# Performance work log

Measured on AMD Instinct MI355X. Metric: run time of the kernel, lower is better.

The kernel has to match this reference:

```python
import jax, jax.numpy as jnp
import numpy as np

B, S, H, I, E, TOP_K = 1, 2048, 1024, 4096, 8, 1


def setup_inputs() -> dict:
    key = jax.random.key(0)
    ks = jax.random.split(key, 8)
    s = 0.02  # init scale for weights
    return {
        "hidden_states": jax.random.normal(ks[0], (B, S, H), jnp.float32),
        "router_w": jax.random.normal(ks[1], (E, H), jnp.float32) * s,
        "w_gate": jax.random.normal(ks[2], (E, I, H), jnp.float32) * s,
        "w_up": jax.random.normal(ks[3], (E, I, H), jnp.float32) * s,
        "w_down": jax.random.normal(ks[4], (E, H, I), jnp.float32) * s,
        "ws_gate": jax.random.normal(ks[5], (I, H), jnp.float32) * s,
        "ws_up": jax.random.normal(ks[6], (I, H), jnp.float32) * s,
        "ws_down": jax.random.normal(ks[7], (H, I), jnp.float32) * s,
    }


def _mlp(x, wg, wu, wd):
    # silu(x @ Wg^T) * (x @ Wu^T) @ Wd^T  (Llama4TextMLP)
    return (jax.nn.silu(x @ wg.T) * (x @ wu.T)) @ wd.T


def reference(hidden_states, router_w, w_gate, w_up, w_down, ws_gate, ws_up, ws_down):
    b, s, h = hidden_states.shape
    hs = hidden_states.reshape(-1, h)                      # [T, H]
    T = hs.shape[0]
    logits = hs @ router_w.T                               # [T, E]
    top_v, top_i = jax.lax.top_k(logits, TOP_K)            # [T, K]
    masked = jnp.full_like(logits, -jnp.inf)
    masked = masked.at[jnp.arange(T)[:, None], top_i].set(top_v)
    scores = jax.nn.sigmoid(masked)                        # [T, E]; sigmoid(-inf)=0

    # In this module every expert sees ALL tokens, scaled by its (mostly-zero) score.
    routed = scores.T[:, :, None] * hs[None, :, :]         # [E, T, H]

    out = _mlp(hs, ws_gate, ws_up, ws_down)                # shared expert, [T, H]
    gate = jnp.einsum('eth,eih->eti', routed, w_gate)      # [E, T, I]
    up = jnp.einsum('eth,eih->eti', routed, w_up)          # [E, T, I]
    expert_out = jnp.einsum('eti,ehi->eth', jax.nn.silu(gate) * up, w_down)
    out = out + expert_out.sum(axis=0)                     # [T, H]
    return out, scores.T                                   # router_scores is [E, T]
```

## Files before the change

### kernel.cpp

```cpp
#include <hip/hip_runtime.h>
#include <hip/hip_bf16.h>
#include <math.h>

#define T_TOK 2048
#define HDIM 1024
#define IDIM 4096
#define NEXP 8
#define RROWS 3200
#define AROWS 5248
#define ZROW  5120
#define NP2   24
#define BK 32

typedef unsigned int uint;
typedef unsigned short ushort;
typedef __attribute__((ext_vector_type(4))) float f32x4;
typedef __attribute__((ext_vector_type(8))) short bf16x8;

__device__ __forceinline__ ushort f2bf(float f) {
  union { float f; uint u; } c; c.f = f;
  uint u = c.u;
  return (ushort)((u + 0x7FFFu + ((u >> 16) & 1u)) >> 16);
}
__device__ __forceinline__ uint cvtpk(float a, float b) {
  uint r;
  asm("v_cvt_pk_bf16_f32 %0, %1, %2" : "=v"(r) : "v"(a), "v"(b));
  return r;
}
__device__ __forceinline__ void gld16(ushort* lds, const ushort* g) {
  __builtin_amdgcn_global_load_lds(
      (const __attribute__((address_space(1))) uint*)g,
      (__attribute__((address_space(3))) uint*)lds, 16, 0, 0);
}
__device__ __forceinline__ int soff(int row, int kc) {
  return ((row >> 4) << 9) + (kc << 7) + ((row & 15) << 3);
}

#define SYNCV(N) { \
  __builtin_amdgcn_sched_barrier(0); \
  asm volatile("s_waitcnt vmcnt(" #N ") lgkmcnt(0)" ::: "memory"); \
  __builtin_amdgcn_s_barrier(); \
  __builtin_amdgcn_sched_barrier(0); }

__global__ __launch_bounds__(256) void router_kernel(
    const float* __restrict__ hs, const float* __restrict__ rw,
    ushort* __restrict__ Xall, float* __restrict__ scores_out,
    int* __restrict__ eidx, float* __restrict__ sval)
{
  const int wave = threadIdx.x >> 6;
  const int lane = threadIdx.x & 63;
  const int t = blockIdx.x * 4 + wave;
  const float* row = hs + (size_t)t * HDIM;
  float v[16];
  #pragma unroll
  for (int i = 0; i < 16; ++i) {
    v[i] = row[lane + 64 * i];
    Xall[(size_t)t * HDIM + lane + 64 * i] = f2bf(v[i]);
  }
  float logit[8];
  #pragma unroll
  for (int e = 0; e < 8; ++e) {
    const float* wr = rw + e * HDIM;
    float s = 0.f;
    #pragma unroll
    for (int i = 0; i < 16; ++i) s += v[i] * wr[lane + 64 * i];
    #pragma unroll
    for (int off = 32; off; off >>= 1) s += __shfl_xor(s, off, 64);
    logit[e] = s;
  }
  if (lane == 0) {
    int be = 0; float bv = logit[0];
    #pragma unroll
    for (int e = 1; e < 8; ++e) if (logit[e] > bv) { bv = logit[e]; be = e; }
    float sc = 1.f / (1.f + expf(-bv));
    eidx[t] = be; sval[t] = sc;
    #pragma unroll
    for (int e = 0; e < 8; ++e) scores_out[(size_t)e * T_TOK + t] = (e == be) ? sc : 0.f;
  }
}

__global__ __launch_bounds__(256) void plan_kernel(
    const int* __restrict__ eidx, int* __restrict__ row2tok, int4* __restrict__ pairs)
{
  __shared__ int cnt[8];
  __shared__ int slot[8];
  const int tid = threadIdx.x;
  if (tid < 8) cnt[tid] = 0;
  __syncthreads();
  for (int t = tid; t < T_TOK; t += 256) atomicAdd(&cnt[eidx[t]], 1);
  __syncthreads();
  if (tid == 0) {
    int np = 0;
    for (int i = 0; i < 8; ++i) pairs[np++] = make_int4(i * 256, i * 256 + 128, -1, 1);
    int o = 0;
    for (int e = 0; e < 8; ++e) {
      slot[e] = o;
      int cap = (cnt[e] + 127) & ~127;
      int nt = cap / 128;
      for (int j = 0; j < nt; j += 2) {
        int ra = T_TOK + o + j * 128;
        int rb = (j + 1 < nt) ? ra + 128 : ZROW;
        pairs[np++] = make_int4(ra, rb, e, 1);
      }
      o += cap;
    }
    for (; np < NP2; ++np) pairs[np] = make_int4(ZROW, ZROW, 0, 0);
  }
  for (int r = tid; r < RROWS; r += 256) row2tok[r] = -1;
  __syncthreads();
  for (int t = tid; t < T_TOK; t += 256) {
    int e = eidx[t];
    int s = atomicAdd(&slot[e], 1);
    row2tok[s] = t;
  }
}

__global__ __launch_bounds__(256) void gather_kernel(
    const float* __restrict__ hs, const int* __restrict__ row2tok,
    const float* __restrict__ sval, ushort* __restrict__ Xall)
{
  const int r = blockIdx.x;
  const int t = row2tok[r];
  const int c0 = threadIdx.x * 4;
  ushort4 o;
  if (t >= 0) {
    const float sc = sval[t];
    float4 v = *(const float4*)(hs + (size_t)t * HDIM + c0);
    o.x = f2bf(sc * v.x); o.y = f2bf(sc * v.y); o.z = f2bf(sc * v.z); o.w = f2bf(sc * v.w);
  } else { o.x = o.y = o.z = o.w = 0; }
  *(ushort4*)(Xall + (size_t)(T_TOK + r) * HDIM + c0) = o;
}

#define LOADB1(S, k0) { \
  gr##S = *(const float4*)(gptr + (k0)); \
  ur##S = *(const float4*)(uptr + (k0)); }

#define WRITEB1(S, B) { \
  *(uint2*)&Bg[B][woff] = make_uint2(cvtpk(gr##S.x, gr##S.y), cvtpk(gr##S.z, gr##S.w)); \
  *(uint2*)&Bu[B][woff] = make_uint2(cvtpk(ur##S.x, ur##S.y), cvtpk(ur##S.z, ur##S.w)); }

#define STAGEA(B, k0) { gld16(&As[B][alds0], asrc0 + (k0)); }

#define READ1(B) \
  bf16x8 af[4], gf[2], uf[2]; \
  _Pragma("unroll") \
  for (int m = 0; m < 4; ++m) af[m] = *(const bf16x8*)&As[B][(wm*4+m)*512 + lp]; \
  _Pragma("unroll") \
  for (int n = 0; n < 2; ++n) { \
    gf[n] = *(const bf16x8*)&Bg[B][(wn*2+n)*512 + lp]; \
    uf[n] = *(const bf16x8*)&Bu[B][(wn*2+n)*512 + lp]; }

#define MFMA1 \
  _Pragma("unroll") \
  for (int m = 0; m < 4; ++m) { \
    _Pragma("unroll") \
    for (int n = 0; n < 2; ++n) { \
      accg[m][n] = __builtin_amdgcn_mfma_f32_16x16x32_bf16(af[m], gf[n], accg[m][n], 0, 0, 0); \
      accu[m][n] = __builtin_amdgcn_mfma_f32_16x16x32_bf16(af[m], uf[n], accu[m][n], 0, 0, 0); } }

__global__ __launch_bounds__(1024, 1) void gemm1_kernel(
    const ushort* __restrict__ Xall,
    const float* __restrict__ w_gate, const float* __restrict__ w_up,
    const float* __restrict__ ws_gate, const float* __restrict__ ws_up,
    const int4* __restrict__ pairs, ushort* __restrict__ actall)
{
  __shared__ __align__(16) ushort As[2][8192];
  __shared__ __align__(16) ushort Bg[2][4096];
  __shared__ __align__(16) ushort Bu[2][4096];

  const int b0 = blockIdx.x;
  const int j = b0 & 7, s = b0 >> 3;
  const int panel = j + 8 * (s / NP2);
  const int4 td = pairs[s % NP2];
  if (td.w == 0) return;
  const int r0a = td.x, r0b = td.y, e = td.z;
  const float* __restrict__ gbase = (e < 0) ? ws_gate : w_gate + (size_t)e * IDIM * HDIM;
  const float* __restrict__ ubase = (e < 0) ? ws_up   : w_up   + (size_t)e * IDIM * HDIM;
  const int col0 = panel * 128;

  const int tid = threadIdx.x;
  const int lane = tid & 63;
  const int w = tid >> 6;
  const int wm = w >> 2, wn = w & 3;

  const int brow = tid >> 3, bch = tid & 7;
  const float* gptr = gbase + (size_t)(col0 + brow) * HDIM + bch * 4;
  const float* uptr = ubase + (size_t)(col0 + brow) * HDIM + bch * 4;
  const int woff = soff(brow, bch >> 1) + (bch & 1) * 4;

  const size_t abs0 = (w < 8) ? (size_t)(r0a + w * 16 + (lane & 15))
                              : (size_t)(r0b + (w - 8) * 16 + (lane & 15));
  const ushort* asrc0 = Xall + abs0 * HDIM + (lane >> 4) * 8;
  const int alds0 = w * 512 + lane * 8;

  float4 gr0, ur0, gr1, ur1;
  const int lp = (lane >> 4) * 128 + (lane & 15) * 8;
  f32x4 accg[4][2] = {};
  f32x4 accu[4][2] = {};

  STAGEA(0, 0);
  __builtin_amdgcn_sched_barrier(0);
  LOADB1(0, 0);
  WRITEB1(0, 0);
  LOADB1(1, BK);
  SYNCV(2);

  const int NS = HDIM / BK;
  for (int kk = 0; kk < NS / 2 - 1; ++kk) {
    const int k = kk * 2;
    {
      READ1(0);
      STAGEA(1, (k + 1) * BK);
      __builtin_amdgcn_sched_barrier(0);
      WRITEB1(1, 1);
      LOADB1(0, (k + 2) * BK);
      MFMA1;
      SYNCV(2);
    }
    {
      READ1(1);
      STAGEA(0, (k + 2) * BK);
      __builtin_amdgcn_sched_barrier(0);
      WRITEB1(0, 0);
      LOADB1(1, (k + 3) * BK);
      MFMA1;
      SYNCV(2);
    }
  }
  {
    READ1(0);
    STAGEA(1, (NS - 1) * BK);
    __builtin_amdgcn_sched_barrier(0);
    WRITEB1(1, 1);
    MFMA1;
    SYNCV(0);
  }
  {
    READ1(1);
    MFMA1;
  }

  const int prbase = wm * 64 + ((lane >> 4) << 2);
  const int cbase = col0 + wn * 32 + (lane & 15);
  #pragma unroll
  for (int m = 0; m < 4; ++m)
    #pragma unroll
    for (int n = 0; n < 2; ++n)
      #pragma unroll
      for (int j2 = 0; j2 < 4; ++j2) {
        const int pr = prbase + m * 16 + j2;
        const size_t ar = (wm < 2) ? (size_t)(r0a + pr) : (size_t)(r0b + pr - 128);
        float g = accg[m][n][j2];
        float u = accu[m][n][j2];
        float sv = g / (1.f + __expf(-g)) * u;
        actall[ar * IDIM + cbase + n * 16] = f2bf(sv);
      }
}

#define LOADB2(S, k0) { br##S = *(const float4*)(bptr + (k0)); }

#define WRITEB2(S, B) { \
  *(uint2*)&Bs[B][woff] = make_uint2(cvtpk(br##S.x, br##S.y), cvtpk(br##S.z, br##S.w)); }

#define READ2(B) \
  bf16x8 af[4], bfr[2]; \
  _Pragma("unroll") \
  for (int m = 0; m < 4; ++m) af[m] = *(const bf16x8*)&As[B][(wm*4+m)*512 + lp]; \
  _Pragma("unroll") \
  for (int n = 0; n < 2; ++n) bfr[n] = *(const bf16x8*)&Bs[B][(wn*2+n)*512 + lp];

#define MFMA2 \
  _Pragma("unroll") \
  for (int m = 0; m < 4; ++m) { \
    _Pragma("unroll") \
    for (int n = 0; n < 2; ++n) \
      acc[m][n] = __builtin_amdgcn_mfma_f32_16x16x32_bf16(af[m], bfr[n], acc[m][n], 0, 0, 0); }

__global__ __launch_bounds__(1024, 1) void gemm2_kernel(
    const ushort* __restrict__ actall,
    const float* __restrict__ w_down, const float* __restrict__ ws_down,
    const int4* __restrict__ pairs, const int* __restrict__ row2tok,
    float* __restrict__ out, float* __restrict__ bufr)
{
  __shared__ __align__(16) ushort As[2][8192];
  __shared__ __align__(16) ushort Bs[2][4096];

  const int b0 = blockIdx.x;
  const int panel = b0 & 7;
  const int4 td = pairs[b0 >> 3];
  if (td.w == 0) return;
  const int r0a = td.x, r0b = td.y, e = td.z;
  const float* __restrict__ bbase = (e < 0) ? ws_down : w_down + (size_t)e * HDIM * IDIM;
  const int col0 = panel * 128;

  const int tid = threadIdx.x;
  const int lane = tid & 63;
  const int w = tid >> 6;
  const int wm = w >> 2, wn = w & 3;

  const int brow = tid >> 3, bch = tid & 7;
  const float* bptr = bbase + (size_t)(col0 + brow) * IDIM + bch * 4;
  const int woff = soff(brow, bch >> 1) + (bch & 1) * 4;

  const size_t abs0 = (w < 8) ? (size_t)(r0a + w * 16 + (lane & 15))
                              : (size_t)(r0b + (w - 8) * 16 + (lane & 15));
  const ushort* asrc0 = actall + abs0 * IDIM + (lane >> 4) * 8;
  const int alds0 = w * 512 + lane * 8;

  float4 br0, br1;
  const int lp = (lane >> 4) * 128 + (lane & 15) * 8;
  f32x4 acc[4][2] = {};

  STAGEA(0, 0);
  __builtin_amdgcn_sched_barrier(0);
  LOADB2(0, 0);
  WRITEB2(0, 0);
  LOADB2(1, BK);
  SYNCV(1);

  const int NS = IDIM / BK;
  for (int kk = 0; kk < NS / 2 - 1; ++kk) {
    const int k = kk * 2;
    {
      READ2(0);
      STAGEA(1, (k + 1) * BK);
      __builtin_amdgcn_sched_barrier(0);
      WRITEB2(1, 1);
      LOADB2(0, (k + 2) * BK);
      MFMA2;
      SYNCV(1);
    }
    {
      READ2(1);
      STAGEA(0, (k + 2) * BK);
      __builtin_amdgcn_sched_barrier(0);
      WRITEB2(0, 0);
      LOADB2(1, (k + 3) * BK);
      MFMA2;
      SYNCV(1);
    }
  }
  {
    READ2(0);
    STAGEA(1, (NS - 1) * BK);
    __builtin_amdgcn_sched_barrier(0);
    WRITEB2(1, 1);
    MFMA2;
    SYNCV(0);
  }
  {
    READ2(1);
    MFMA2;
  }

  const int prbase = wm * 64 + ((lane >> 4) << 2);
  const int cbase = col0 + wn * 32 + (lane & 15);
  #pragma unroll
  for (int m = 0; m < 4; ++m)
    #pragma unroll
    for (int j2 = 0; j2 < 4; ++j2) {
      const int pr = prbase + m * 16 + j2;
      const int ar = (wm < 2) ? (r0a + pr) : (r0b + pr - 128);
      if (e < 0) {
        #pragma unroll
        for (int n = 0; n < 2; ++n)
          out[(size_t)ar * HDIM + cbase + n * 16] = acc[m][n][j2];
      } else {
        const int t = row2tok[ar - T_TOK];
        if (t >= 0) {
          #pragma unroll
          for (int n = 0; n < 2; ++n)
            bufr[(size_t)t * HDIM + cbase + n * 16] = acc[m][n][j2];
        }
      }
    }
}

__global__ __launch_bounds__(256) void add_kernel(
    float* __restrict__ out, const float* __restrict__ bufr)
{
  const size_t i = ((size_t)blockIdx.x * 256 + threadIdx.x) * 4;
  float4 a = *(float4*)(out + i);
  const float4 b = *(const float4*)(bufr + i);
  a.x += b.x; a.y += b.y; a.z += b.z; a.w += b.w;
  *(float4*)(out + i) = a;
}

extern "C" void kernel_launch(void* const* d_in, const int* in_sizes, int n_in,
                              void* d_out, int out_size, void* d_ws, size_t ws_size,
                              hipStream_t stream)
{
  const float* hs      = (const float*)d_in[0];
  const float* rw      = (const float*)d_in[1];
  const float* w_gate  = (const float*)d_in[2];
  const float* w_up    = (const float*)d_in[3];
  const float* w_down  = (const float*)d_in[4];
  const float* ws_gate = (const float*)d_in[5];
  const float* ws_up   = (const float*)d_in[6];
  const float* ws_down = (const float*)d_in[7];

  float* out = (float*)d_out;
  float* scores_out = out + (size_t)T_TOK * HDIM;

  char* ws = (char*)d_ws;
  ushort* Xall   = (ushort*)ws;
  ushort* actall = (ushort*)(ws + 10747904);
  float*  bufr   = (float*)(ws + 53739520);
  int*    eidx   = (int*)(ws + 62128128);
  float*  sval   = (float*)(ws + 62136320);
  int*    r2t    = (int*)(ws + 62144512);
  int4*   pairs  = (int4*)(ws + 62157312);

  router_kernel<<<T_TOK / 4, 256, 0, stream>>>(hs, rw, Xall, scores_out, eidx, sval);
  plan_kernel<<<1, 256, 0, stream>>>(eidx, r2t, pairs);
  gather_kernel<<<RROWS, 256, 0, stream>>>(hs, r2t, sval, Xall);
  gemm1_kernel<<<(IDIM / 128) * NP2, 1024, 0, stream>>>(
      Xall, w_gate, w_up, ws_gate, ws_up, pairs, actall);
  gemm2_kernel<<<(HDIM / 128) * NP2, 1024, 0, stream>>>(
      actall, w_down, ws_down, pairs, r2t, out, bufr);
  add_kernel<<<(T_TOK * HDIM) / 1024, 256, 0, stream>>>(out, bufr);
}
```

Baseline: 329.1 us.

## Triple-buffer A tiles in LDS and prefetch two stages ahead

```diff
diff --git a/kernel.cpp b/kernel.cpp
--- a/kernel.cpp
+++ b/kernel.cpp
@@ -139,12 +139,12 @@
   *(uint2*)&Bg[B][woff] = make_uint2(cvtpk(gr##S.x, gr##S.y), cvtpk(gr##S.z, gr##S.w)); \
   *(uint2*)&Bu[B][woff] = make_uint2(cvtpk(ur##S.x, ur##S.y), cvtpk(ur##S.z, ur##S.w)); }
 
-#define STAGEA(B, k0) { gld16(&As[B][alds0], asrc0 + (k0)); }
-
-#define READ1(B) \
+#define STAGEA(ABASE, k0) { gld16((ABASE) + alds0, asrc0 + (k0)); }
+
+#define READ1(ABASE, B) \
   bf16x8 af[4], gf[2], uf[2]; \
   _Pragma("unroll") \
-  for (int m = 0; m < 4; ++m) af[m] = *(const bf16x8*)&As[B][(wm*4+m)*512 + lp]; \
+  for (int m = 0; m < 4; ++m) af[m] = *(const bf16x8*)((ABASE) + (wm*4+m)*512 + lp); \
   _Pragma("unroll") \
   for (int n = 0; n < 2; ++n) { \
     gf[n] = *(const bf16x8*)&Bg[B][(wn*2+n)*512 + lp]; \
@@ -158,13 +158,15 @@
       accg[m][n] = __builtin_amdgcn_mfma_f32_16x16x32_bf16(af[m], gf[n], accg[m][n], 0, 0, 0); \
       accu[m][n] = __builtin_amdgcn_mfma_f32_16x16x32_bf16(af[m], uf[n], accu[m][n], 0, 0, 0); } }
 
+#define ROTA { ushort* aT_ = aR; aR = aM; aM = aS; aS = aT_; }
+
 __global__ __launch_bounds__(1024, 1) void gemm1_kernel(
     const ushort* __restrict__ Xall,
     const float* __restrict__ w_gate, const float* __restrict__ w_up,
     const float* __restrict__ ws_gate, const float* __restrict__ ws_up,
     const int4* __restrict__ pairs, ushort* __restrict__ actall)
 {
-  __shared__ __align__(16) ushort As[2][8192];
+  __shared__ __align__(16) ushort As[3][8192];
   __shared__ __align__(16) ushort Bg[2][4096];
   __shared__ __align__(16) ushort Bu[2][4096];
 
@@ -193,50 +195,53 @@
   const ushort* asrc0 = Xall + abs0 * HDIM + (lane >> 4) * 8;
   const int alds0 = w * 512 + lane * 8;
 
+  ushort* aR = &As[0][0];
+  ushort* aM = &As[1][0];
+  ushort* aS = &As[2][0];
+
   float4 gr0, ur0, gr1, ur1;
   const int lp = (lane >> 4) * 128 + (lane & 15) * 8;
   f32x4 accg[4][2] = {};
   f32x4 accu[4][2] = {};
 
-  STAGEA(0, 0);
-  __builtin_amdgcn_sched_barrier(0);
+  STAGEA(aR, 0);
   LOADB1(0, 0);
+  STAGEA(aM, BK);
+  LOADB1(1, BK);
   WRITEB1(0, 0);
-  LOADB1(1, BK);
-  SYNCV(2);
+  SYNCV(3);
 
   const int NS = HDIM / BK;
   for (int kk = 0; kk < NS / 2 - 1; ++kk) {
     const int k = kk * 2;
     {
-      READ1(0);
-      STAGEA(1, (k + 1) * BK);
-      __builtin_amdgcn_sched_barrier(0);
-      WRITEB1(1, 1);
+      READ1(aR, 0);
+      STAGEA(aS, (k + 2) * BK);
       LOADB1(0, (k + 2) * BK);
       MFMA1;
-      SYNCV(2);
+      WRITEB1(1, 1);
+      SYNCV(3);
+      ROTA;
     }
     {
-      READ1(1);
-      STAGEA(0, (k + 2) * BK);
-      __builtin_amdgcn_sched_barrier(0);
-      WRITEB1(0, 0);
+      READ1(aR, 1);
+      STAGEA(aS, (k + 3) * BK);
       LOADB1(1, (k + 3) * BK);
       MFMA1;
-      SYNCV(2);
+      WRITEB1(0, 0);
+      SYNCV(3);
+      ROTA;
     }
   }
   {
-    READ1(0);
-    STAGEA(1, (NS - 1) * BK);
-    __builtin_amdgcn_sched_barrier(0);
+    READ1(aR, 0);
+    MFMA1;
     WRITEB1(1, 1);
-    MFMA1;
     SYNCV(0);
+    ROTA;
   }
   {
-    READ1(1);
+    READ1(aR, 1);
     MFMA1;
   }
 
@@ -262,10 +267,10 @@
 #define WRITEB2(S, B) { \
   *(uint2*)&Bs[B][woff] = make_uint2(cvtpk(br##S.x, br##S.y), cvtpk(br##S.z, br##S.w)); }
 
-#define READ2(B) \
+#define READ2(ABASE, B) \
   bf16x8 af[4], bfr[2]; \
   _Pragma("unroll") \
-  for (int m = 0; m < 4; ++m) af[m] = *(const bf16x8*)&As[B][(wm*4+m)*512 + lp]; \
+  for (int m = 0; m < 4; ++m) af[m] = *(const bf16x8*)((ABASE) + (wm*4+m)*512 + lp); \
   _Pragma("unroll") \
   for (int n = 0; n < 2; ++n) bfr[n] = *(const bf16x8*)&Bs[B][(wn*2+n)*512 + lp];
 
@@ -282,7 +287,7 @@
     const int4* __restrict__ pairs, const int* __restrict__ row2tok,
     float* __restrict__ out, float* __restrict__ bufr)
 {
-  __shared__ __align__(16) ushort As[2][8192];
+  __shared__ __align__(16) ushort As[3][8192];
   __shared__ __align__(16) ushort Bs[2][4096];
 
   const int b0 = blockIdx.x;
@@ -307,49 +312,52 @@
   const ushort* asrc0 = actall + abs0 * IDIM + (lane >> 4) * 8;
   const int alds0 = w * 512 + lane * 8;
 
+  ushort* aR = &As[0][0];
+  ushort* aM = &As[1][0];
+  ushort* aS = &As[2][0];
+
   float4 br0, br1;
   const int lp = (lane >> 4) * 128 + (lane & 15) * 8;
   f32x4 acc[4][2] = {};
 
-  STAGEA(0, 0);
-  __builtin_amdgcn_sched_barrier(0);
+  STAGEA(aR, 0);
   LOADB2(0, 0);
+  STAGEA(aM, BK);
+  LOADB2(1, BK);
   WRITEB2(0, 0);
-  LOADB2(1, BK);
-  SYNCV(1);
+  SYNCV(2);
 
   const int NS = IDIM / BK;
   for (int kk = 0; kk < NS / 2 - 1; ++kk) {
     const int k = kk * 2;
     {
-      READ2(0);
-      STAGEA(1, (k + 1) * BK);
-      __builtin_amdgcn_sched_barrier(0);
-      WRITEB2(1, 1);
+      READ2(aR, 0);
+      STAGEA(aS, (k + 2) * BK);
       LOADB2(0, (k + 2) * BK);
       MFMA2;
-      SYNCV(1);
+      WRITEB2(1, 1);
+      SYNCV(2);
+      ROTA;
     }
     {
-      READ2(1);
-      STAGEA(0, (k + 2) * BK);
-      __builtin_amdgcn_sched_barrier(0);
-      WRITEB2(0, 0);
+      READ2(aR, 1);
+      STAGEA(aS, (k + 3) * BK);
       LOADB2(1, (k + 3) * BK);
       MFMA2;
-      SYNCV(1);
+      WRITEB2(0, 0);
+      SYNCV(2);
+      ROTA;
     }
   }
   {
-    READ2(0);
-    STAGEA(1, (NS - 1) * BK);
-    __builtin_amdgcn_sched_barrier(0);
+    READ2(aR, 0);
+    MFMA2;
     WRITEB2(1, 1);
-    MFMA2;
     SYNCV(0);
+    ROTA;
   }
   {
-    READ2(1);
+    READ2(aR, 1);
     MFMA2;
   }
 
```

Result: faster. 308.6 us (-6.2%).
